# Kernel optimization log

Hardware: AMD Instinct MI355X
Metric: run time of the kernel (lower is better)

The kernel has to match this reference:

```python
import jax, jax.numpy as jnp
import numpy as np

FOCUS = 3  # focusing_factor
EPS = 1e-6


def setup_inputs() -> dict:
    key = jax.random.key(0)
    ks = jax.random.split(key, 6)
    B, N, C = 4, 4096, 1024
    s = 0.02
    return {
        "x": jax.random.normal(ks[0], (B, N, C), jnp.float32),
        "w_qkv": jax.random.normal(ks[1], (3 * C, C), jnp.float32) * s,
        "w_proj": jax.random.normal(ks[2], (C, C), jnp.float32) * s,
        "b_proj": jax.random.normal(ks[3], (C,), jnp.float32) * s,
        "w_dwc": jax.random.normal(ks[4], (C, 3), jnp.float32) * s,
        "b_dwc": jax.random.normal(ks[5], (C,), jnp.float32) * s,
    }


def _norm_last(t):
    return t / jnp.sum(t, axis=-1, keepdims=True)


def reference(x, w_qkv, w_proj, b_proj, w_dwc, b_dwc):
    B, N, C = x.shape
    H = 16
    d = C // H
    # qkv projection -> (3, B, H, N, d)
    qkv = jnp.einsum('bnc,oc->bno', x, w_qkv).reshape(B, N, 3, H, d)
    qkv = jnp.transpose(qkv, (2, 0, 3, 1, 4))
    q, k, v = qkv[0], qkv[1], qkv[2]
    # focused kernel feature map: relu -> l1 norm -> power -> renorm
    q = _norm_last(jax.nn.relu(q) + EPS)
    k = _norm_last(jax.nn.relu(k) + EPS)
    q = _norm_last(q ** FOCUS)
    k = _norm_last(k ** FOCUS)
    # linear attention
    kv = jnp.einsum('bhnd,bhne->bhde', k, v)                     # (B,H,d,d)
    z = 1.0 / (jnp.einsum('bhnd,bhd->bhn', q, k.sum(axis=2)) + EPS)
    out = jnp.einsum('bhnd,bhde,bhn->bhne', q, kv, z)            # (B,H,N,d)
    out = jnp.transpose(out, (0, 2, 1, 3)).reshape(B, N, C)
    # depthwise conv1d over sequence, kernel=3, padding=1 (torch layout [C,1,3])
    xp = jnp.pad(out, ((0, 0), (1, 1), (0, 0)))
    conv = (xp[:, 0:N, :] * w_dwc[:, 0]
            + xp[:, 1:N + 1, :] * w_dwc[:, 1]
            + xp[:, 2:N + 2, :] * w_dwc[:, 2]) + b_dwc
    out = out + conv
    # output projection (dropout is identity in eval)
    return jnp.einsum('bnc,oc->bno', out, w_proj) + b_proj
```

## Files before the change

### kernel.cpp

```cpp
#include <hip/hip_runtime.h>
#include <hip/hip_bf16.h>

#define BB 4
#define NN 4096
#define CC 1024
#define HH 16
#define MM (BB*NN)
#define EPSF 1e-6f

typedef _Float16 f16x8 __attribute__((ext_vector_type(8)));
typedef float f32x4 __attribute__((ext_vector_type(4)));

__device__ __forceinline__ void gload_lds16(const void* g, void* l) {
    __builtin_amdgcn_global_load_lds(
        (const __attribute__((address_space(1))) void*)g,
        (__attribute__((address_space(3))) void*)l, 16, 0, 0);
}

__global__ __launch_bounds__(256)
void tofp16_all(const float* __restrict__ x, const float* __restrict__ wq,
                const float* __restrict__ wp, _Float16* __restrict__ xf,
                _Float16* __restrict__ wqf, _Float16* __restrict__ wpf)
{
    int i = blockIdx.x * 256 + threadIdx.x;
    const float* src; _Float16* dst; int off;
    if (i < 4194304)      { src = x;  dst = xf;  off = 0; }
    else if (i < 4980736) { src = wq; dst = wqf; off = 4194304; }
    else                  { src = wp; dst = wpf; off = 4980736; }
    int j = i - off;
    float4 f = ((const float4*)src)[j];
    short4 pk;
    pk.x = __builtin_bit_cast(short, (_Float16)f.x);
    pk.y = __builtin_bit_cast(short, (_Float16)f.y);
    pk.z = __builtin_bit_cast(short, (_Float16)f.z);
    pk.w = __builtin_bit_cast(short, (_Float16)f.w);
    ((short4*)dst)[j] = pk;
}


#define STAGE(BUF, KT) do {                                                           \
    gload_lds16(gA0 + (KT) * 32, (char*)lds + (BUF) * 24576 + tid * 16);              \
    gload_lds16(gB0 + (KT) * 32, (char*)lds + (BUF) * 24576 + 8192 + tid * 16);       \
    gload_lds16(gB1 + (KT) * 32, (char*)lds + (BUF) * 24576 + 16384 + tid * 16);      \
} while (0)

#define TILE(KT, CUR, NXT, DOSTAGE, VMSTR) do {                                      \
    if (DOSTAGE) STAGE(NXT, (KT) + 2);                                               \
    const char* Ab_ = (const char*)lds + (CUR) * 24576 + aoff;                       \
    const char* Bb_ = (const char*)lds + (CUR) * 24576 + 8192 + boff;                \
    f16x8 af_[4], bf_[4];                                                            \
    _Pragma("unroll")                                                                \
    for (int m_ = 0; m_ < 4; ++m_) af_[m_] = *(const f16x8*)(Ab_ + m_ * 1024);       \
    _Pragma("unroll")                                                                \
    for (int n_ = 0; n_ < 4; ++n_) bf_[n_] = *(const f16x8*)(Bb_ + n_ * 1024);       \
    __builtin_amdgcn_s_setprio(1);                                                   \
    _Pragma("unroll")                                                                \
    for (int m_ = 0; m_ < 4; ++m_)                                                   \
    _Pragma("unroll")                                                                \
    for (int n_ = 0; n_ < 4; ++n_)                                                   \
        acc[m_][n_] = __builtin_amdgcn_mfma_f32_16x16x32_f16(af_[m_], bf_[n_],       \
                                                             acc[m_][n_], 0, 0, 0); \
    __builtin_amdgcn_s_setprio(0);                                                   \
    asm volatile("s_waitcnt " VMSTR ::: "memory");                                   \
    __builtin_amdgcn_s_barrier();                                                    \
    __builtin_amdgcn_sched_barrier(0);                                               \
} while (0)

template<int EPI>
__global__ __launch_bounds__(512, 4)
void gemm128(const _Float16* __restrict__ A, const _Float16* __restrict__ Bm,
             void* __restrict__ Cout, _Float16* __restrict__ Kt,
             _Float16* __restrict__ Vt, const float* __restrict__ bias,
             const int Ncols, const int gx)
{
    __shared__ _Float16 lds[3 * 12288];

    const int tid  = threadIdx.x;
    const int lane = tid & 63;
    const int wid  = tid >> 6;
    const int wm   = wid >> 2;
    const int wn   = wid & 3;

    const int nwg = gridDim.x;
    const int wg  = blockIdx.x;
    const int sw  = (wg & 7) * (nwg >> 3) + (wg >> 3);
    const int by  = sw / gx, bx = sw - by * gx;
    const int brow = by << 7, bcol = bx << 8;

    const int sr = tid >> 2;
    const int sc8 = (tid & 3) ^ ((sr >> 1) & 3);
    const _Float16* gA0 = A  + (size_t)(brow + sr) * 1024 + sc8 * 8;
    const _Float16* gB0 = Bm + (size_t)(bcol + sr) * 1024 + sc8 * 8;
    const _Float16* gB1 = gB0 + (size_t)128 * 1024;

    const int l15 = lane & 15, q = lane >> 4;
    const int swz  = ((q ^ ((l15 >> 1) & 3)) << 4);
    const int aoff = (wm * 64 + l15) * 64 + swz;
    const int boff = (wn * 64 + l15) * 64 + swz;

    f32x4 acc[4][4] = {};

    STAGE(0, 0);
    STAGE(1, 1);
    asm volatile("s_waitcnt vmcnt(3)" ::: "memory");
    __builtin_amdgcn_s_barrier();
    __builtin_amdgcn_sched_barrier(0);

#pragma unroll 1
    for (int tt = 0; tt < 30; tt += 3) {
        TILE(tt,     0, 2, 1, "vmcnt(3)");
        TILE(tt + 1, 1, 0, 1, "vmcnt(3)");
        TILE(tt + 2, 2, 1, 1, "vmcnt(3)");
    }
    TILE(30, 0, 2, 0, "vmcnt(0)");
    TILE(31, 1, 0, 0, "vmcnt(0)");

    if (EPI == 0) {
        const int sec = bcol >> 10;
        const bool feat = (sec < 2);
        if (feat) {
#pragma unroll
            for (int m = 0; m < 4; ++m)
#pragma unroll
                for (int r = 0; r < 4; ++r) {
                    float u[4]; float ssum = 0.f;
#pragma unroll
                    for (int n = 0; n < 4; ++n) {
                        float uu = fmaxf(acc[m][n][r], 0.f) + EPSF;
                        float c = uu * uu * uu;
                        u[n] = c; ssum += c;
                    }
                    ssum += __shfl_xor(ssum, 1, 16);
                    ssum += __shfl_xor(ssum, 2, 16);
                    ssum += __shfl_xor(ssum, 4, 16);
                    ssum += __shfl_xor(ssum, 8, 16);
                    float inv = 1.0f / ssum;
#pragma unroll
                    for (int n = 0; n < 4; ++n) acc[m][n][r] = u[n] * inv;
                }
        }
        if (sec == 0) {
            _Float16* Qh = (_Float16*)Cout;
            const int b  = brow >> 12;
            const int h  = ((bcol & 1023) >> 6) + wn;
            const size_t qb = (size_t)(b * 16 + h) * 4096;
            const int n0 = (brow & 4095) + wm * 64;
#pragma unroll
            for (int m = 0; m < 4; ++m) {
                int nr = n0 + m * 16 + q * 4;
#pragma unroll
                for (int r = 0; r < 4; ++r) {
                    size_t base = (qb + nr + r) * 64 + l15;
#pragma unroll
                    for (int n = 0; n < 4; ++n)
                        Qh[base + n * 16] = (_Float16)acc[m][n][r];
                }
            }
        } else {
            _Float16* T = (sec == 1) ? Kt : Vt;
            const int b   = brow >> 12;
            const int hb  = ((bcol & 1023) >> 6) + wn;
            const int bh  = b * 16 + hb;
            const int n0  = (brow & 4095) + wm * 64;
            char* st = (char*)lds + wid * 8704;
#pragma unroll
            for (int m = 0; m < 4; ++m) {
                int tokc = m * 16 + q * 4;
#pragma unroll
                for (int n = 0; n < 4; ++n) {
                    short4 pk;
                    pk.x = __builtin_bit_cast(short, (_Float16)acc[m][n][0]);
                    pk.y = __builtin_bit_cast(short, (_Float16)acc[m][n][1]);
                    pk.z = __builtin_bit_cast(short, (_Float16)acc[m][n][2]);
                    pk.w = __builtin_bit_cast(short, (_Float16)acc[m][n][3]);
                    int dk = n * 16 + l15;
                    *(short4*)(st + dk * 136 + tokc * 2) = pk;
                }
            }
#pragma unroll
            for (int it = 0; it < 16; ++it) {
                int dk = it * 4 + q;
                short4 v4 = *(const short4*)(st + dk * 136 + l15 * 8);
                *(short4*)(T + ((size_t)(bh * 64 + dk)) * 4096 + n0 + l15 * 4) = v4;
            }
        }
    } else {
        float* Oc = (float*)Cout;
        const int colb = bcol + wn * 64 + l15;
#pragma unroll
        for (int m = 0; m < 4; ++m) {
            int rb = brow + wm * 64 + m * 16 + q * 4;
#pragma unroll
            for (int r = 0; r < 4; ++r) {
                size_t base = (size_t)(rb + r) * Ncols + colb;
#pragma unroll
                for (int n = 0; n < 4; ++n)
                    Oc[base + n * 16] = acc[m][n][r] + bias[colb + n * 16];
            }
        }
    }
}

__global__ __launch_bounds__(256)
void kv_mfma(const _Float16* __restrict__ Kt, const _Float16* __restrict__ Vt,
             float* __restrict__ kvp, float* __restrict__ ksump)
{
    __shared__ float red[4][64][64];
    __shared__ float ksr[4][64];
    int bx = blockIdx.x;
    int bh = bx >> 2, kseg = bx & 3;
    int tid = threadIdx.x;
    int w = tid >> 6, lane = tid & 63, p = lane & 15, q = lane >> 4;
    const _Float16* Vb = Vt + (size_t)bh * 64 * 4096;
    const _Float16* Kb = Kt + (size_t)bh * 64 * 4096;
    f32x4 acc[4][4] = {};
    float ksp[4] = {0.f, 0.f, 0.f, 0.f};
    int kbase = kseg * 1024 + w * 256 + q * 8;
#pragma unroll 1
    for (int ks = 0; ks < 8; ++ks) {
        int kb = kbase + ks * 32;
        f16x8 af[4], bf[4];
#pragma unroll
        for (int m = 0; m < 4; ++m)
            af[m] = *(const f16x8*)(Vb + (size_t)(m * 16 + p) * 4096 + kb);
#pragma unroll
        for (int n = 0; n < 4; ++n) {
            bf[n] = *(const f16x8*)(Kb + (size_t)(n * 16 + p) * 4096 + kb);
#pragma unroll
            for (int j = 0; j < 8; ++j) ksp[n] += (float)bf[n][j];
        }
#pragma unroll
        for (int m = 0; m < 4; ++m)
#pragma unroll
            for (int n = 0; n < 4; ++n)
                acc[m][n] = __builtin_amdgcn_mfma_f32_16x16x32_f16(
                    af[m], bf[n], acc[m][n], 0, 0, 0);
    }
#pragma unroll
    for (int n = 0; n < 4; ++n) {
        ksp[n] += __shfl_xor(ksp[n], 16);
        ksp[n] += __shfl_xor(ksp[n], 32);
    }
    if (q == 0)
#pragma unroll
        for (int n = 0; n < 4; ++n) ksr[w][n * 16 + p] = ksp[n];
#pragma unroll
    for (int m = 0; m < 4; ++m)
#pragma unroll
        for (int n = 0; n < 4; ++n)
            *(f32x4*)&red[w][n * 16 + p][m * 16 + q * 4] = acc[m][n];
    __syncthreads();
    int dv = tid & 63, dkb = (tid >> 6) * 16;
    float* ko = kvp + ((size_t)(kseg * 64 + bh)) * 4096;
    f32x4 o[4];
#pragma unroll
    for (int i = 0; i < 16; ++i) {
        float s = red[0][dkb + i][dv] + red[1][dkb + i][dv]
                + red[2][dkb + i][dv] + red[3][dkb + i][dv];
        o[i >> 2][i & 3] = s;
    }
#pragma unroll
    for (int i = 0; i < 4; ++i)
        *(f32x4*)(ko + dv * 64 + dkb + i * 4) = o[i];
    if (tid < 64)
        ksump[(size_t)(kseg * 64 + bh) * 64 + tid] =
            ksr[0][tid] + ksr[1][tid] + ksr[2][tid] + ksr[3][tid];
}

__global__ __launch_bounds__(256)
void kv_reduce(const float* __restrict__ kvp, const float* __restrict__ ksump,
               _Float16* __restrict__ kvT)
{
    int idx = blockIdx.x * 256 + threadIdx.x;
    int col = idx & 63;
    int t = idx >> 6;
    int bh = t / 80;
    int row = t - bh * 80;
    float s = 0.f;
    if (row < 64) {
        int src = bh * 4096 + row * 64 + col;
        s = kvp[src] + kvp[262144 + src] + kvp[2 * 262144 + src] + kvp[3 * 262144 + src];
    } else if (row == 64) {
        int src = bh * 64 + col;
        s = ksump[src] + ksump[4096 + src] + ksump[2 * 4096 + src] + ksump[3 * 4096 + src];
    }
    kvT[idx] = (_Float16)s;
}

__global__ __launch_bounds__(256)
void attn_conv(const _Float16* __restrict__ Qh, const _Float16* __restrict__ kvT,
               const float* __restrict__ wdwc, const float* __restrict__ bdwc,
               _Float16* __restrict__ yf)
{
    __shared__ _Float16 ybuf[258][68];
    int blk = blockIdx.x;
    int b = blk >> 8, h = (blk >> 4) & 15, chunk = blk & 15;
    int bh = b * 16 + h;
    int tid = threadIdx.x, w = tid >> 6, lane = tid & 63, p = lane & 15, q = lane >> 4;
    const _Float16* kvb = kvT + (size_t)bh * (80 * 64);
    const _Float16* Qb  = Qh + (size_t)bh * 4096 * 64;
    f16x8 bf[2][5];
#pragma unroll
    for (int kst = 0; kst < 2; ++kst)
#pragma unroll
        for (int n = 0; n < 5; ++n)
            bf[kst][n] = *(const f16x8*)(kvb + (n * 16 + p) * 64 + kst * 32 + q * 8);

    int tok0 = chunk * 256 + w * 64;

    f32x4 acc[4][5] = {};
#pragma unroll
    for (int kst = 0; kst < 2; ++kst) {
        f16x8 af[4];
#pragma unroll
        for (int m = 0; m < 4; ++m)
            af[m] = *(const f16x8*)(Qb + (size_t)(tok0 + m * 16 + p) * 64 + kst * 32 + q * 8);
#pragma unroll
        for (int m = 0; m < 4; ++m)
#pragma unroll
            for (int n = 0; n < 5; ++n)
                acc[m][n] = __builtin_amdgcn_mfma_f32_16x16x32_f16(
                    af[m], bf[kst][n], acc[m][n], 0, 0, 0);
    }
#pragma unroll
    for (int m = 0; m < 4; ++m)
#pragma unroll
        for (int r = 0; r < 4; ++r) {
            float sz = __shfl(acc[m][4][r], lane & 48);
            float zz = 1.0f / (sz + EPSF);
            int row = 1 + w * 64 + m * 16 + q * 4 + r;
#pragma unroll
            for (int n = 0; n < 4; ++n)
                ybuf[row][n * 16 + p] = (_Float16)(acc[m][n][r] * zz);
        }
    if (w == 0 || w == 3) {
        bool lo = (w == 0);
        bool live = lo ? (chunk > 0) : (chunk < 15);
        float val = 0.f;
        if (live) {
            int t = lo ? (chunk * 256 - 1) : (chunk * 256 + 256);
            float sd = 0.f, sz = 0.f;
#pragma unroll
            for (int i = 0; i < 8; ++i) {
                f16x8 qq = *(const f16x8*)(Qb + (size_t)t * 64 + i * 8);
                f16x8 kk = *(const f16x8*)(kvb + lane * 64 + i * 8);
                f16x8 ks = *(const f16x8*)(kvb + 64 * 64 + i * 8);
#pragma unroll
                for (int j = 0; j < 8; ++j) {
                    sd += (float)qq[j] * (float)kk[j];
                    sz += (float)qq[j] * (float)ks[j];
                }
            }
            val = sd / (sz + EPSF);
        }
        ybuf[lo ? 0 : 257][lane] = (_Float16)val;
    }
    __syncthreads();
    int dv = lane;
    int c = h * 64 + dv;
    float w0 = wdwc[c * 3 + 0], w1 = wdwc[c * 3 + 1], w2 = wdwc[c * 3 + 2];
    float bb = bdwc[c];
#pragma unroll 4
    for (int it = 0; it < 64; ++it) {
        int tok = it * 4 + w;
        float ym = (float)ybuf[tok][dv];
        float yc = (float)ybuf[tok + 1][dv];
        float yp = (float)ybuf[tok + 2][dv];
        float val = yc + w0 * ym + w1 * yc + w2 * yp + bb;
        yf[((size_t)(b * 4096 + chunk * 256 + tok)) * 1024 + c] = (_Float16)val;
    }
}

extern "C" void kernel_launch(void* const* d_in, const int* in_sizes, int n_in,
                              void* d_out, int out_size, void* d_ws, size_t ws_size,
                              hipStream_t stream)
{
    const float* x      = (const float*)d_in[0];
    const float* w_qkv  = (const float*)d_in[1];
    const float* w_proj = (const float*)d_in[2];
    const float* b_proj = (const float*)d_in[3];
    const float* w_dwc  = (const float*)d_in[4];
    const float* b_dwc  = (const float*)d_in[5];

    char* p = (char*)d_ws;
    _Float16* xf   = (_Float16*)p;  p += (size_t)MM * CC * 2;
    _Float16* wqf  = (_Float16*)p;  p += (size_t)3 * CC * CC * 2;
    _Float16* wpf  = (_Float16*)p;  p += (size_t)CC * CC * 2;
    _Float16* Qh   = (_Float16*)p;  p += (size_t)MM * CC * 2;
    _Float16* Kt   = (_Float16*)p;  p += (size_t)64 * 64 * NN * 2;
    _Float16* Vt   = (_Float16*)p;  p += (size_t)64 * 64 * NN * 2;
    float*    kvp  = (float*)p;     p += (size_t)4 * 64 * 4096 * 4;
    float*    ksump= (float*)p;     p += (size_t)4 * 64 * 64 * 4;
    _Float16* kvT  = (_Float16*)p;  p += (size_t)64 * 80 * 64 * 2;
    _Float16* yf   = (_Float16*)p;  p += (size_t)MM * CC * 2;

    tofp16_all<<<20480, 256, 0, stream>>>(x, w_qkv, w_proj, xf, wqf, wpf);

    gemm128<0><<<dim3(12 * 128), 512, 0, stream>>>(
        xf, wqf, (void*)Qh, Kt, Vt, nullptr, 3072, 12);

    kv_mfma<<<256, 256, 0, stream>>>(Kt, Vt, kvp, ksump);
    kv_reduce<<<1280, 256, 0, stream>>>(kvp, ksump, kvT);

    attn_conv<<<BB * HH * 16, 256, 0, stream>>>(Qh, kvT, w_dwc, b_dwc, yf);

    gemm128<1><<<dim3(4 * 128), 512, 0, stream>>>(
        yf, wpf, d_out, nullptr, nullptr, b_proj, 1024, 4);
}
```

Before: 223.0 us.

## Replace 128x256 GEMM with 256x256 tile, 8-phase interleaved LDS pipeline

Both GEMMs switch from a 128x256 tile with a K-step of 32 and triple buffering to a 256x256 tile with a K-step of 64, double-buffered in 128KB of LDS. Each K-tile is split into four MFMA phases with barriers between them, and global-to-LDS loads for the next tile are issued between the phases. The goal is to raise arithmetic intensity per LDS byte and hide global loads behind MFMA work. In exchange, occupancy drops to one workgroup per CU, the grid is halved, and the extra barriers add synchronisation overhead.

```diff
diff --git a/kernel.cpp b/kernel.cpp
--- a/kernel.cpp
+++ b/kernel.cpp
@@ -38,42 +38,81 @@
 }
 
 
-#define STAGE(BUF, KT) do {                                                           \
-    gload_lds16(gA0 + (KT) * 32, (char*)lds + (BUF) * 24576 + tid * 16);              \
-    gload_lds16(gB0 + (KT) * 32, (char*)lds + (BUF) * 24576 + 8192 + tid * 16);       \
-    gload_lds16(gB1 + (KT) * 32, (char*)lds + (BUF) * 24576 + 16384 + tid * 16);      \
+#define BAR   __builtin_amdgcn_s_barrier()
+#define LGKM0 do { asm volatile("s_waitcnt lgkmcnt(0)" ::: "memory"); \
+                   __builtin_amdgcn_sched_barrier(0); } while(0)
+
+#define STAGE_A(H, BUF, TT) do {                                                      \
+    gload_lds16(gA0 + (size_t)(H) * 131072 + (TT) * 64,                               \
+                (char*)lds + (BUF) * 65536 + (H) * 16384 + tid * 16);                 \
+    gload_lds16(gA0 + (size_t)(H) * 131072 + 65536 + (TT) * 64,                       \
+                (char*)lds + (BUF) * 65536 + (H) * 16384 + 8192 + tid * 16);          \
 } while (0)
-
-#define TILE(KT, CUR, NXT, DOSTAGE, VMSTR) do {                                      \
-    if (DOSTAGE) STAGE(NXT, (KT) + 2);                                               \
-    const char* Ab_ = (const char*)lds + (CUR) * 24576 + aoff;                       \
-    const char* Bb_ = (const char*)lds + (CUR) * 24576 + 8192 + boff;                \
-    f16x8 af_[4], bf_[4];                                                            \
-    _Pragma("unroll")                                                                \
-    for (int m_ = 0; m_ < 4; ++m_) af_[m_] = *(const f16x8*)(Ab_ + m_ * 1024);       \
-    _Pragma("unroll")                                                                \
-    for (int n_ = 0; n_ < 4; ++n_) bf_[n_] = *(const f16x8*)(Bb_ + n_ * 1024);       \
-    __builtin_amdgcn_s_setprio(1);                                                   \
-    _Pragma("unroll")                                                                \
-    for (int m_ = 0; m_ < 4; ++m_)                                                   \
-    _Pragma("unroll")                                                                \
-    for (int n_ = 0; n_ < 4; ++n_)                                                   \
-        acc[m_][n_] = __builtin_amdgcn_mfma_f32_16x16x32_f16(af_[m_], bf_[n_],       \
-                                                             acc[m_][n_], 0, 0, 0); \
-    __builtin_amdgcn_s_setprio(0);                                                   \
-    asm volatile("s_waitcnt " VMSTR ::: "memory");                                   \
-    __builtin_amdgcn_s_barrier();                                                    \
-    __builtin_amdgcn_sched_barrier(0);                                               \
+#define STAGE_B(H, BUF, TT) do {                                                      \
+    gload_lds16(gB0 + (size_t)(H) * 131072 + (TT) * 64,                               \
+                (char*)lds + (BUF) * 65536 + 32768 + (H) * 16384 + tid * 16);         \
+    gload_lds16(gB0 + (size_t)(H) * 131072 + 65536 + (TT) * 64,                       \
+                (char*)lds + (BUF) * 65536 + 32768 + (H) * 16384 + 8192 + tid * 16);  \
 } while (0)
 
+#define MFMA16(MB, NB, AF, BF) do {                                                   \
+    __builtin_amdgcn_s_setprio(1);                                                    \
+    _Pragma("unroll") for (int kk_ = 0; kk_ < 2; ++kk_)                               \
+    _Pragma("unroll") for (int m_ = 0; m_ < 4; ++m_)                                  \
+    _Pragma("unroll") for (int n_ = 0; n_ < 2; ++n_)                                  \
+        acc[(MB) + m_][(NB) + n_] = __builtin_amdgcn_mfma_f32_16x16x32_f16(           \
+            AF[kk_][m_], BF[kk_][n_], acc[(MB) + m_][(NB) + n_], 0, 0, 0);            \
+    __builtin_amdgcn_s_setprio(0);                                                    \
+} while (0)
+
+#define KTILE(BUF, TT, S1, S2, S3, S4, DOVM, VMN) do {                                \
+    const char* Ar_ = (const char*)lds + (BUF) * 65536 + wm * 16384;                  \
+    const char* Br_ = (const char*)lds + (BUF) * 65536 + 32768 + (wn >> 1) * 16384;   \
+    f16x8 af_[2][4], b0_[2][2], b1_[2][2];                                            \
+                                        \
+    _Pragma("unroll") for (int kk_ = 0; kk_ < 2; ++kk_) {                             \
+        _Pragma("unroll") for (int m_ = 0; m_ < 4; ++m_)                              \
+            af_[kk_][m_] = *(const f16x8*)(Ar_ + m_ * 2048 + aoff[kk_]);              \
+        _Pragma("unroll") for (int n_ = 0; n_ < 2; ++n_)                              \
+            b0_[kk_][n_] = *(const f16x8*)(Br_ + n_ * 2048 + boff[kk_]);              \
+    }                                                                                 \
+    if (S1) STAGE_A(0, (BUF) ^ 1, (TT) + 1);                                          \
+    BAR; LGKM0;                                                                       \
+    MFMA16(0, 0, af_, b0_);                                                           \
+    BAR;                                                                              \
+                                                 \
+    _Pragma("unroll") for (int kk_ = 0; kk_ < 2; ++kk_)                               \
+        _Pragma("unroll") for (int n_ = 0; n_ < 2; ++n_)                              \
+            b1_[kk_][n_] = *(const f16x8*)(Br_ + (2 + n_) * 2048 + boff[kk_]);        \
+    if (S2) STAGE_A(1, (BUF) ^ 1, (TT) + 1);                                          \
+    BAR; LGKM0;                                                                       \
+    MFMA16(0, 2, af_, b1_);                                                           \
+    BAR;                                                                              \
+                                                 \
+    _Pragma("unroll") for (int kk_ = 0; kk_ < 2; ++kk_)                               \
+        _Pragma("unroll") for (int m_ = 0; m_ < 4; ++m_)                              \
+            af_[kk_][m_] = *(const f16x8*)(Ar_ + (4 + m_) * 2048 + aoff[kk_]);        \
+    if (S3) STAGE_B(0, (BUF), (TT) + 2);                                              \
+    BAR; LGKM0;                                                                       \
+    MFMA16(4, 0, af_, b0_);                                                           \
+    BAR;                                                                              \
+                                \
+    if (S4) STAGE_B(1, (BUF), (TT) + 2);                                              \
+    if (DOVM) { asm volatile("s_waitcnt vmcnt(" #VMN ")" ::: "memory");               \
+                __builtin_amdgcn_sched_barrier(0); }                                  \
+    BAR;                                                                              \
+    MFMA16(4, 2, af_, b1_);                                                           \
+    BAR;                                                                              \
+} while (0)
+
 template<int EPI>
-__global__ __launch_bounds__(512, 4)
-void gemm128(const _Float16* __restrict__ A, const _Float16* __restrict__ Bm,
-             void* __restrict__ Cout, _Float16* __restrict__ Kt,
-             _Float16* __restrict__ Vt, const float* __restrict__ bias,
-             const int Ncols, const int gx)
-{
-    __shared__ _Float16 lds[3 * 12288];
+__global__ __launch_bounds__(512, 1)
+void gemm8p(const _Float16* __restrict__ A, const _Float16* __restrict__ Bm,
+            void* __restrict__ Cout, _Float16* __restrict__ Kt,
+            _Float16* __restrict__ Vt, const float* __restrict__ bias,
+            const int Ncols, const int gx)
+{
+    __shared__ _Float16 lds[65536];
 
     const int tid  = threadIdx.x;
     const int lane = tid & 63;
@@ -85,42 +124,44 @@
     const int wg  = blockIdx.x;
     const int sw  = (wg & 7) * (nwg >> 3) + (wg >> 3);
     const int by  = sw / gx, bx = sw - by * gx;
-    const int brow = by << 7, bcol = bx << 8;
-
-    const int sr = tid >> 2;
-    const int sc8 = (tid & 3) ^ ((sr >> 1) & 3);
-    const _Float16* gA0 = A  + (size_t)(brow + sr) * 1024 + sc8 * 8;
-    const _Float16* gB0 = Bm + (size_t)(bcol + sr) * 1024 + sc8 * 8;
-    const _Float16* gB1 = gB0 + (size_t)128 * 1024;
-
-    const int l15 = lane & 15, q = lane >> 4;
-    const int swz  = ((q ^ ((l15 >> 1) & 3)) << 4);
-    const int aoff = (wm * 64 + l15) * 64 + swz;
-    const int boff = (wn * 64 + l15) * 64 + swz;
-
-    f32x4 acc[4][4] = {};
-
-    STAGE(0, 0);
-    STAGE(1, 1);
-    asm volatile("s_waitcnt vmcnt(3)" ::: "memory");
-    __builtin_amdgcn_s_barrier();
+    const int brow = by << 8, bcol = bx << 8;
+
+    const int sr  = tid >> 3;
+    const int sch = (tid & 7) ^ (sr & 7);
+    const _Float16* gA0 = A  + (size_t)(brow + sr) * 1024 + sch * 8;
+    const _Float16* gB0 = Bm + (size_t)(bcol + sr) * 1024 + sch * 8;
+
+    const int l15 = lane & 15, q = lane >> 4, s3 = lane & 7;
+    int aoff[2], boff[2];
+#pragma unroll
+    for (int kk = 0; kk < 2; ++kk) {
+        int ch = ((kk << 2) | q) ^ s3;
+        aoff[kk] = l15 * 128 + ch * 16;
+        boff[kk] = ((wn & 1) * 64 + l15) * 128 + ch * 16;
+    }
+
+    f32x4 acc[8][4] = {};
+
+    STAGE_A(0, 0, 0); STAGE_A(1, 0, 0); STAGE_B(0, 0, 0); STAGE_B(1, 0, 0);
+    STAGE_B(0, 1, 1); STAGE_B(1, 1, 1);
+    asm volatile("s_waitcnt vmcnt(4)" ::: "memory");
     __builtin_amdgcn_sched_barrier(0);
+    BAR;
 
 #pragma unroll 1
-    for (int tt = 0; tt < 30; tt += 3) {
-        TILE(tt,     0, 2, 1, "vmcnt(3)");
-        TILE(tt + 1, 1, 0, 1, "vmcnt(3)");
-        TILE(tt + 2, 2, 1, 1, "vmcnt(3)");
-    }
-    TILE(30, 0, 2, 0, "vmcnt(0)");
-    TILE(31, 1, 0, 0, "vmcnt(0)");
+    for (int t = 0; t < 14; t += 2) {
+        KTILE(0, t,     1, 1, 1, 1, 1, 4);
+        KTILE(1, t + 1, 1, 1, 1, 1, 1, 4);
+    }
+    KTILE(0, 14, 1, 1, 0, 0, 1, 0);
+    KTILE(1, 15, 0, 0, 0, 0, 0, 0);
 
     if (EPI == 0) {
         const int sec = bcol >> 10;
         const bool feat = (sec < 2);
         if (feat) {
 #pragma unroll
-            for (int m = 0; m < 4; ++m)
+            for (int m = 0; m < 8; ++m)
 #pragma unroll
                 for (int r = 0; r < 4; ++r) {
                     float u[4]; float ssum = 0.f;
@@ -142,11 +183,11 @@
         if (sec == 0) {
             _Float16* Qh = (_Float16*)Cout;
             const int b  = brow >> 12;
-            const int h  = ((bcol & 1023) >> 6) + wn;
+            const int h  = (bcol >> 6) + wn;
             const size_t qb = (size_t)(b * 16 + h) * 4096;
-            const int n0 = (brow & 4095) + wm * 64;
-#pragma unroll
-            for (int m = 0; m < 4; ++m) {
+            const int n0 = (brow & 4095) + wm * 128;
+#pragma unroll
+            for (int m = 0; m < 8; ++m) {
                 int nr = n0 + m * 16 + q * 4;
 #pragma unroll
                 for (int r = 0; r < 4; ++r) {
@@ -161,35 +202,39 @@
             const int b   = brow >> 12;
             const int hb  = ((bcol & 1023) >> 6) + wn;
             const int bh  = b * 16 + hb;
-            const int n0  = (brow & 4095) + wm * 64;
+            const int n0  = (brow & 4095) + wm * 128;
             char* st = (char*)lds + wid * 8704;
 #pragma unroll
-            for (int m = 0; m < 4; ++m) {
-                int tokc = m * 16 + q * 4;
-#pragma unroll
-                for (int n = 0; n < 4; ++n) {
-                    short4 pk;
-                    pk.x = __builtin_bit_cast(short, (_Float16)acc[m][n][0]);
-                    pk.y = __builtin_bit_cast(short, (_Float16)acc[m][n][1]);
-                    pk.z = __builtin_bit_cast(short, (_Float16)acc[m][n][2]);
-                    pk.w = __builtin_bit_cast(short, (_Float16)acc[m][n][3]);
-                    int dk = n * 16 + l15;
-                    *(short4*)(st + dk * 136 + tokc * 2) = pk;
+            for (int c2 = 0; c2 < 2; ++c2) {
+#pragma unroll
+                for (int m = 0; m < 4; ++m) {
+                    int mm = c2 * 4 + m;
+                    int tokc = m * 16 + q * 4;
+#pragma unroll
+                    for (int n = 0; n < 4; ++n) {
+                        short4 pk;
+                        pk.x = __builtin_bit_cast(short, (_Float16)acc[mm][n][0]);
+                        pk.y = __builtin_bit_cast(short, (_Float16)acc[mm][n][1]);
+                        pk.z = __builtin_bit_cast(short, (_Float16)acc[mm][n][2]);
+                        pk.w = __builtin_bit_cast(short, (_Float16)acc[mm][n][3]);
+                        int dk = n * 16 + l15;
+                        *(short4*)(st + dk * 136 + tokc * 2) = pk;
+                    }
                 }
-            }
-#pragma unroll
-            for (int it = 0; it < 16; ++it) {
-                int dk = it * 4 + q;
-                short4 v4 = *(const short4*)(st + dk * 136 + l15 * 8);
-                *(short4*)(T + ((size_t)(bh * 64 + dk)) * 4096 + n0 + l15 * 4) = v4;
+#pragma unroll
+                for (int it = 0; it < 16; ++it) {
+                    int dk = it * 4 + q;
+                    short4 v4 = *(const short4*)(st + dk * 136 + l15 * 8);
+                    *(short4*)(T + ((size_t)(bh * 64 + dk)) * 4096 + n0 + c2 * 64 + l15 * 4) = v4;
+                }
             }
         }
     } else {
         float* Oc = (float*)Cout;
         const int colb = bcol + wn * 64 + l15;
 #pragma unroll
-        for (int m = 0; m < 4; ++m) {
-            int rb = brow + wm * 64 + m * 16 + q * 4;
+        for (int m = 0; m < 8; ++m) {
+            int rb = brow + wm * 128 + m * 16 + q * 4;
 #pragma unroll
             for (int r = 0; r < 4; ++r) {
                 size_t base = (size_t)(rb + r) * Ncols + colb;
@@ -396,7 +441,7 @@
 
     tofp16_all<<<20480, 256, 0, stream>>>(x, w_qkv, w_proj, xf, wqf, wpf);
 
-    gemm128<0><<<dim3(12 * 128), 512, 0, stream>>>(
+    gemm8p<0><<<dim3(12 * 64), 512, 0, stream>>>(
         xf, wqf, (void*)Qh, Kt, Vt, nullptr, 3072, 12);
 
     kv_mfma<<<256, 256, 0, stream>>>(Kt, Vt, kvp, ksump);
@@ -404,6 +449,6 @@
 
     attn_conv<<<BB * HH * 16, 256, 0, stream>>>(Qh, kvT, w_dwc, b_dwc, yf);
 
-    gemm128<1><<<dim3(4 * 128), 512, 0, stream>>>(
+    gemm8p<1><<<dim3(4 * 64), 512, 0, stream>>>(
         yf, wpf, d_out, nullptr, nullptr, b_proj, 1024, 4);
 }
```

Measured after the change: 219.9 us. About the same (-1.4%).
